# Kernel optimization log

Measured on AMD Instinct MI355X. Metric: run time of the kernel, lower is better.

Reference implementation:

```python
import jax, jax.numpy as jnp
import numpy as np

BOS = 1
MAX_LEN = 20


def _lstm_cell(x, h, c, Wih, Whh, bih, bhh):
    # torch.nn.LSTMCell gate order: i, f, g, o
    g = x @ Wih.T + h @ Whh.T + bih + bhh
    i, f, gg, o = jnp.split(g, 4, axis=-1)
    c = jax.nn.sigmoid(f) * c + jax.nn.sigmoid(i) * jnp.tanh(gg)
    h = jax.nn.sigmoid(o) * jnp.tanh(c)
    return h, c


def setup_inputs() -> dict:
    key = jax.random.key(0)
    ks = jax.random.split(key, 12)
    B, K, D = 512, 36, 2048
    A, H, Em, V = 512, 512, 300, 10000
    s = 0.02
    rn = lambda k, shape, sc=s: sc * jax.random.normal(k, shape, dtype=jnp.float32)
    return {
        'feats': jax.random.normal(ks[0], (B, K, D), dtype=jnp.float32),
        'Wp': rn(ks[1], (A, D)), 'bp': jnp.zeros((A,), jnp.float32),
        'E': rn(ks[2], (V, Em), 0.1).at[0].set(0.0),  # padding_idx = 0
        'Wih1': rn(ks[3], (4 * H, Em + A)), 'Whh1': rn(ks[4], (4 * H, H)),
        'bih1': jnp.zeros((4 * H,), jnp.float32), 'bhh1': jnp.zeros((4 * H,), jnp.float32),
        'Wih2': rn(ks[5], (4 * H, H + A)), 'Whh2': rn(ks[6], (4 * H, H)),
        'bih2': jnp.zeros((4 * H,), jnp.float32), 'bhh2': jnp.zeros((4 * H,), jnp.float32),
        'Wa1': rn(ks[7], (A, H + A)), 'ba1': jnp.zeros((A,), jnp.float32),
        'wa2': rn(ks[8], (1, A)), 'ba2': jnp.zeros((1,), jnp.float32),
        'Wo': rn(ks[9], (V, H)), 'bo': jnp.zeros((V,), jnp.float32),
    }


def reference(feats, Wp, bp, E, Wih1, Whh1, bih1, bhh1, Wih2, Whh2, bih2, bhh2,
              Wa1, ba1, wa2, ba2, Wo, bo):
    B, K, D = feats.shape
    H = Whh1.shape[1]
    f_att = feats @ Wp.T + bp                      # [B, K, A]
    f_mean = f_att.mean(axis=1)                    # [B, A]
    # attn Linear over concat([h1, f_att]): split columns, precompute f_att term
    Wa1_h, Wa1_f = Wa1[:, :H], Wa1[:, H:]
    att_f = f_att @ Wa1_f.T + ba1                  # [B, K, A]
    x0 = jnp.broadcast_to(E[BOS], (B, E.shape[1]))
    z = jnp.zeros((B, H), jnp.float32)
    carry0 = (x0, z, z, z, z)

    def step(carry, _):
        x, h1, c1, h2, c2 = carry
        h1, c1 = _lstm_cell(jnp.concatenate([x, f_mean], axis=-1), h1, c1,
                            Wih1, Whh1, bih1, bhh1)
        pre = jnp.tanh(att_f + (h1 @ Wa1_h.T)[:, None, :])   # [B, K, A]
        e = pre @ wa2[0] + ba2[0]                            # [B, K]
        alpha = jax.nn.softmax(e, axis=-1)
        ctx = jnp.einsum('bk,bka->ba', alpha, f_att)         # [B, A]
        h2, c2 = _lstm_cell(jnp.concatenate([h1, ctx], axis=-1), h2, c2,
                            Wih2, Whh2, bih2, bhh2)
        logit = h2 @ Wo.T + bo                               # [B, V]  (dropout is identity in eval)
        nxt = jnp.argmax(logit, axis=-1)
        return (E[nxt], h1, c1, h2, c2), nxt

    _, ids = jax.lax.scan(step, carry0, None, length=MAX_LEN - 1)
    return ids.T  # [B, MAX_LEN-1], matches torch.stack(out_ids, 1)
```

## Files before the change

kernel.cpp:

```cpp
#include <hip/hip_runtime.h>
#include <math.h>
#include <stdint.h>

constexpr int Bsz = 512, Kf = 36, Dd = 2048, Aa = 512, Hh = 512, Em = 300;
constexpr int Vv = 10000, TSTEPS = 19, BOS = 1;
constexpr int K1 = 832;
constexpr int K2 = 1536;
constexpr int VvP = 10112;
constexpr int NTL = VvP / 64;
constexpr float SPLIT_S  = 2048.0f;
constexpr float SPLIT_IS = 1.0f / 2048.0f;

#define CDIV(a,b) (((a)+(b)-1)/(b))

typedef _Float16 f16x8 __attribute__((ext_vector_type(8)));
typedef float    f32x4 __attribute__((ext_vector_type(4)));

typedef const unsigned int GU __attribute__((address_space(1)));
typedef unsigned int       LU __attribute__((address_space(3)));

__device__ __forceinline__ void gload16(const void* g, void* l) {
    __builtin_amdgcn_global_load_lds((GU*)g, (LU*)l, 16, 0, 0);
}

template<int N> __device__ __forceinline__ void wait_vm() {
    if constexpr (N == 0)       asm volatile("s_waitcnt vmcnt(0)" ::: "memory");
    else if constexpr (N == 4)  asm volatile("s_waitcnt vmcnt(4)" ::: "memory");
    else if constexpr (N == 6)  asm volatile("s_waitcnt vmcnt(6)" ::: "memory");
    else if constexpr (N == 8)  asm volatile("s_waitcnt vmcnt(8)" ::: "memory");
    else static_assert(N == 0, "unsupported vmcnt literal");
}
#define WAIT_LGKM asm volatile("s_waitcnt lgkmcnt(0)" ::: "memory")
#define SB0 __builtin_amdgcn_sched_barrier(0)
#define BAR __builtin_amdgcn_s_barrier()

__device__ __forceinline__ float sigm(float v) { return 1.0f / (1.0f + expf(-v)); }

__device__ __forceinline__ void wsplit(_Float16* __restrict__ hi, _Float16* __restrict__ lo,
                                       size_t idx, float v) {
    _Float16 h = (_Float16)v;
    hi[idx] = h;
    lo[idx] = (_Float16)((v - (float)h) * SPLIT_S);
}

template<int BM, int BN, int BK, bool AF32, bool SWZ, int OCC, int EPI>
__global__ __launch_bounds__(256, OCC)
void gemm_sp(const float* __restrict__ Af,
             const _Float16* __restrict__ Ahi, const _Float16* __restrict__ Alo, int lda,
             const _Float16* __restrict__ Bhi, const _Float16* __restrict__ Blo, int ldb,
             float* __restrict__ C, int ldc, int N, int K,
             const float* __restrict__ bias1, const float* __restrict__ bias2,
             const float* __restrict__ addC, int gxn,
             float* __restrict__ candV, int* __restrict__ candI, int ntl)
{
    constexpr int WM = BM / 2, WN = BN / 2;
    constexpr int MF = WM / 16, NF = WN / 16;
    constexpr int PA  = BK / 8;
    constexpr int PSA = BM * 8 + 8;
    constexpr int PSB = BN * 8 + 8;
    constexpr int SZA = PA * PSA, SZB = PA * PSB;
    constexpr int OAH = 0, OAL = SZA, OBH = 2 * SZA, OBL = 2 * SZA + SZB;
    constexpr int BUF = 2 * SZA + 2 * SZB;
    constexpr int NCHA = BM * BK / 2048;
    constexpr int NCHB = BN * BK / 2048;
    constexpr int LW = 2 * NCHA + 2 * NCHB;
    __shared__ _Float16 sm[2 * BUF];

    int mt, nt;
    if constexpr (SWZ) {
        const int nwg = gridDim.x;
        const int cpx = nwg >> 3;
        const int orig = blockIdx.x;
        const int lid = (orig & 7) * cpx + (orig >> 3);
        nt = lid % gxn; mt = lid / gxn;
    } else {
        nt = blockIdx.x; mt = blockIdx.y;
    }
    const int m0 = mt * BM, n0 = nt * BN;

    const int t    = threadIdx.x;
    const int lane = t & 63;
    const int w    = t >> 6;
    const int wr   = w >> 1, wc = w & 1;
    const int l15  = lane & 15, l4 = lane >> 4;

    f32x4 acch[MF][NF];
    f32x4 accm[MF][NF];
    #pragma unroll
    for (int m = 0; m < MF; ++m)
        #pragma unroll
        for (int n = 0; n < NF; ++n) {
            acch[m][n] = (f32x4){0.f, 0.f, 0.f, 0.f};
            accm[m][n] = (f32x4){0.f, 0.f, 0.f, 0.f};
        }

    const int nkt = K / BK;

    auto stageB = [&](int bufo, int kt) {
        #pragma unroll
        for (int i = 0; i < NCHB; ++i) {
            const int q  = i * 256 + t;
            const int p  = q / BN, r = q % BN;
            const int qw = i * 256 + (t & ~63);
            const int pu = qw / BN, ru = qw % BN;
            const size_t goff = (size_t)(n0 + r) * ldb + kt * BK + p * 8;
            gload16(Bhi + goff, &sm[bufo + OBH + pu * PSB + ru * 8]);
            gload16(Blo + goff, &sm[bufo + OBL + pu * PSB + ru * 8]);
        }
    };
    auto stageA16 = [&](int bufo, int kt) {
        #pragma unroll
        for (int i = 0; i < NCHA; ++i) {
            const int q  = i * 256 + t;
            const int p  = q / BM, r = q % BM;
            const int qw = i * 256 + (t & ~63);
            const int pu = qw / BM, ru = qw % BM;
            const size_t goff = (size_t)(m0 + r) * lda + kt * BK + p * 8;
            gload16(Ahi + goff, &sm[bufo + OAH + pu * PSA + ru * 8]);
            gload16(Alo + goff, &sm[bufo + OAL + pu * PSA + ru * 8]);
        }
    };
    auto issueA = [&](float4 (&rd)[NCHA][2], int kt) {
        #pragma unroll
        for (int i = 0; i < NCHA; ++i) {
            const int q = i * 256 + t;
            const int p = q / BM, r = q % BM;
            const float* src = Af + (size_t)(m0 + r) * lda + kt * BK + p * 8;
            rd[i][0] = *(const float4*)src;
            rd[i][1] = *(const float4*)(src + 4);
        }
    };
    auto writeA = [&](int bufo, float4 (&rd)[NCHA][2]) {
        #pragma unroll
        for (int i = 0; i < NCHA; ++i) {
            const int q = i * 256 + t;
            const int p = q / BM, r = q % BM;
            const float f[8] = {rd[i][0].x, rd[i][0].y, rd[i][0].z, rd[i][0].w,
                                rd[i][1].x, rd[i][1].y, rd[i][1].z, rd[i][1].w};
            f16x8 hi, lo;
            #pragma unroll
            for (int j = 0; j < 8; ++j) {
                _Float16 h = (_Float16)f[j];
                hi[j] = h;
                lo[j] = (_Float16)((f[j] - (float)h) * SPLIT_S);
            }
            *(f16x8*)&sm[bufo + OAH + p * PSA + r * 8] = hi;
            *(f16x8*)&sm[bufo + OAL + p * PSA + r * 8] = lo;
        }
    };
    auto compute = [&](int bufo) {
        #pragma unroll
        for (int s = 0; s < BK / 32; ++s) {
            f16x8 ah[MF], al[MF], bh[NF], bl[NF];
            const int pl = s * 4 + l4;
            #pragma unroll
            for (int m = 0; m < MF; ++m) {
                const int row = wr * WM + m * 16 + l15;
                ah[m] = *(const f16x8*)&sm[bufo + OAH + pl * PSA + row * 8];
                al[m] = *(const f16x8*)&sm[bufo + OAL + pl * PSA + row * 8];
            }
            #pragma unroll
            for (int n = 0; n < NF; ++n) {
                const int row = wc * WN + n * 16 + l15;
                bh[n] = *(const f16x8*)&sm[bufo + OBH + pl * PSB + row * 8];
                bl[n] = *(const f16x8*)&sm[bufo + OBL + pl * PSB + row * 8];
            }
            #pragma unroll
            for (int m = 0; m < MF; ++m)
                #pragma unroll
                for (int n = 0; n < NF; ++n) {
                    acch[m][n] = __builtin_amdgcn_mfma_f32_16x16x32_f16(ah[m], bh[n], acch[m][n], 0, 0, 0);
                    accm[m][n] = __builtin_amdgcn_mfma_f32_16x16x32_f16(ah[m], bl[n], accm[m][n], 0, 0, 0);
                    accm[m][n] = __builtin_amdgcn_mfma_f32_16x16x32_f16(al[m], bh[n], accm[m][n], 0, 0, 0);
                }
        }
    };

    if constexpr (AF32) {
        float4 rA[NCHA][2], rB[NCHA][2];
        issueA(rA, 0); stageB(0, 0);
        for (int kt = 0; kt < nkt; kt += 2) {
            issueA(rB, kt + 1); stageB(BUF, kt + 1);
            wait_vm<LW>(); SB0;
            writeA(0, rA);
            WAIT_LGKM; SB0;
            BAR; SB0;
            compute(0);
            SB0; WAIT_LGKM; BAR; SB0;
            if (kt + 2 < nkt) { issueA(rA, kt + 2); stageB(0, kt + 2); wait_vm<LW>(); }
            else              { wait_vm<0>(); }
            SB0;
            writeA(BUF, rB);
            WAIT_LGKM; SB0;
            BAR; SB0;
            compute(BUF);
            SB0; WAIT_LGKM; BAR; SB0;
        }
    } else {
        stageA16(0, 0); stageB(0, 0);
        for (int kt = 0; kt < nkt; ++kt) {
            const int bufc = (kt & 1) ? BUF : 0;
            const int bufn = BUF - bufc;
            if (kt + 1 < nkt) { stageA16(bufn, kt + 1); stageB(bufn, kt + 1); wait_vm<LW>(); }
            else              { wait_vm<0>(); }
            SB0;
            BAR; SB0;
            compute(bufc);
            SB0; WAIT_LGKM; BAR; SB0;
        }
    }

    if constexpr (EPI == 0) {
        #pragma unroll
        for (int m = 0; m < MF; ++m) {
            const int rowb = m0 + wr * WM + m * 16 + l4 * 4;
            #pragma unroll
            for (int n = 0; n < NF; ++n) {
                const int col = n0 + wc * WN + n * 16 + l15;
                if (col < N) {
                    float bb = 0.f;
                    if (bias1) bb += bias1[col];
                    if (bias2) bb += bias2[col];
                    #pragma unroll
                    for (int r = 0; r < 4; ++r) {
                        const size_t idx = (size_t)(rowb + r) * ldc + col;
                        float v = acch[m][n][r] + accm[m][n][r] * SPLIT_IS + bb;
                        if (addC) v += addC[idx];
                        C[idx] = v;
                    }
                }
            }
        }
    } else {
        float* sEv = reinterpret_cast<float*>(&sm[0]);
        int*   sEi = reinterpret_cast<int*>(&sm[0]) + 2 * BM;
        float bv[MF][4];
        int   bix[MF][4];
        #pragma unroll
        for (int m = 0; m < MF; ++m)
            #pragma unroll
            for (int r = 0; r < 4; ++r) { bv[m][r] = -INFINITY; bix[m][r] = 0x7fffffff; }
        #pragma unroll
        for (int m = 0; m < MF; ++m)
            #pragma unroll
            for (int r = 0; r < 4; ++r)
                #pragma unroll
                for (int n = 0; n < NF; ++n) {
                    const int col = n0 + wc * WN + n * 16 + l15;
                    if (col < N) {
                        const float x = acch[m][n][r] + accm[m][n][r] * SPLIT_IS + bias1[col];
                        if (x > bv[m][r]) { bv[m][r] = x; bix[m][r] = col; }
                    }
                }
        #pragma unroll
        for (int mask = 1; mask < 16; mask <<= 1) {
            #pragma unroll
            for (int m = 0; m < MF; ++m)
                #pragma unroll
                for (int r = 0; r < 4; ++r) {
                    const float ov = __shfl_xor(bv[m][r], mask);
                    const int   oi = __shfl_xor(bix[m][r], mask);
                    if (ov > bv[m][r] || (ov == bv[m][r] && oi < bix[m][r])) {
                        bv[m][r] = ov; bix[m][r] = oi;
                    }
                }
        }
        if (l15 == 0) {
            #pragma unroll
            for (int m = 0; m < MF; ++m)
                #pragma unroll
                for (int r = 0; r < 4; ++r) {
                    const int rl = wr * WM + m * 16 + l4 * 4 + r;
                    sEv[wc * BM + rl] = bv[m][r];
                    sEi[wc * BM + rl] = bix[m][r];
                }
        }
        __syncthreads();
        if (t < BM) {
            float v0 = sEv[t]; int i0 = sEi[t];
            const float v1 = sEv[BM + t]; const int i1 = sEi[BM + t];
            if (v1 > v0 || (v1 == v0 && i1 < i0)) { v0 = v1; i0 = i1; }
            candV[(size_t)(m0 + t) * ntl + nt] = v0;
            candI[(size_t)(m0 + t) * ntl + nt] = i0;
        }
    }
}

__global__ __launch_bounds__(256)
void split_convert(const float* __restrict__ src, int srcld, int validR,
                   _Float16* __restrict__ dhi, _Float16* __restrict__ dlo,
                   int dstld, int coloff, int R, int C)
{
    const int total = R * C;
    for (int i = blockIdx.x * 256 + threadIdx.x; i < total; i += gridDim.x * 256) {
        const int r = i / C, c = i % C;
        const float v = (r < validR) ? src[(size_t)r * srcld + c] : 0.f;
        wsplit(dhi, dlo, (size_t)r * dstld + coloff + c, v);
    }
}

__global__ __launch_bounds__(256)
void init_kernel(_Float16* __restrict__ a1h, _Float16* __restrict__ a1l,
                 _Float16* __restrict__ a2h, _Float16* __restrict__ a2l,
                 float* __restrict__ c1, float* __restrict__ c2,
                 const float* __restrict__ E)
{
    const int idx = blockIdx.x * 256 + threadIdx.x;
    if (idx < Bsz * K1) {
        const int col = idx % K1;
        const float v = (col < Em) ? E[(size_t)BOS * Em + col] : 0.f;
        wsplit(a1h, a1l, idx, v);
    }
    if (idx < Bsz * K2) wsplit(a2h, a2l, idx, 0.f);
    if (idx < Bsz * Hh) { c1[idx] = 0.f; c2[idx] = 0.f; }
}

__global__ __launch_bounds__(256)
void fmean_kernel(const float* __restrict__ f_att, float* __restrict__ f_mean,
                  _Float16* __restrict__ fmh, _Float16* __restrict__ fml)
{
    const int b = blockIdx.x;
    for (int a = threadIdx.x; a < Aa; a += 256) {
        float s = 0.f;
        for (int k = 0; k < Kf; ++k) s += f_att[((size_t)b * Kf + k) * Aa + a];
        const float v = s * (1.0f / 36.0f);
        f_mean[(size_t)b * Aa + a] = v;
        wsplit(fmh, fml, (size_t)b * Aa + a, v);
    }
}

__global__ __launch_bounds__(256)
void lstm_cell_kernel(const float* __restrict__ g, float* __restrict__ c,
                      _Float16* __restrict__ hhi, _Float16* __restrict__ hlo,
                      int hld, int hoff,
                      _Float16* __restrict__ h2hi, _Float16* __restrict__ h2lo,
                      int h2ld, int h2off)
{
    const int idx = blockIdx.x * 256 + threadIdx.x;
    const int b = idx >> 9, h = idx & 511;
    const float* gb = g + (size_t)b * 2048;
    const float gi = gb[h], gf = gb[512 + h], gc = gb[1024 + h], go = gb[1536 + h];
    const float cv = sigm(gf) * c[idx] + sigm(gi) * tanhf(gc);
    c[idx] = cv;
    const float hv = sigm(go) * tanhf(cv);
    wsplit(hhi, hlo, (size_t)b * hld + hoff + h, hv);
    if (h2hi) wsplit(h2hi, h2lo, (size_t)b * h2ld + h2off + h, hv);
}

__global__ __launch_bounds__(256)
void attn_fused(const float* __restrict__ att_f, const float* __restrict__ q,
                const float* __restrict__ wa2, const float* __restrict__ ba2,
                const float* __restrict__ f_att,
                _Float16* __restrict__ a2h, _Float16* __restrict__ a2l)
{
    const int b = blockIdx.x, tid = threadIdx.x;
    const int w = tid >> 6, lane = tid & 63;
    __shared__ float se[Kf];
    __shared__ float wk[Kf];
    const float* pq = q + (size_t)b * Aa;
    for (int k = w; k < Kf; k += 4) {
        const float* pf = att_f + ((size_t)b * Kf + k) * Aa;
        float s = 0.f;
        #pragma unroll
        for (int j = 0; j < Aa; j += 64) {
            const int a = j + lane;
            s += tanhf(pf[a] + pq[a]) * wa2[a];
        }
        #pragma unroll
        for (int off = 32; off; off >>= 1) s += __shfl_down(s, off);
        if (lane == 0) se[k] = s + ba2[0];
    }
    __syncthreads();
    if (tid < Kf) {
        float mx = -INFINITY;
        for (int k = 0; k < Kf; ++k) mx = fmaxf(mx, se[k]);
        float ssum = 0.f;
        for (int k = 0; k < Kf; ++k) ssum += expf(se[k] - mx);
        wk[tid] = expf(se[tid] - mx) / ssum;
    }
    __syncthreads();
    for (int a = tid; a < Aa; a += 256) {
        float acc = 0.f;
        for (int k = 0; k < Kf; ++k)
            acc = fmaf(wk[k], f_att[((size_t)b * Kf + k) * Aa + a], acc);
        wsplit(a2h, a2l, (size_t)b * K2 + Hh + a, acc);
    }
}

__global__ __launch_bounds__(256)
void argmax_embed_kernel(const float* __restrict__ candV, const int* __restrict__ candI,
                         const float* __restrict__ E,
                         _Float16* __restrict__ a1h, _Float16* __restrict__ a1l,
                         int* __restrict__ out, int t, int ntl)
{
    const int b = blockIdx.x;
    const int tid = threadIdx.x;
    __shared__ float sv[256];
    __shared__ int   si[256];
    float bvv = -INFINITY; int bii = 0x7fffffff;
    if (tid < ntl) { bvv = candV[(size_t)b * ntl + tid]; bii = candI[(size_t)b * ntl + tid]; }
    sv[tid] = bvv; si[tid] = bii;
    __syncthreads();
    for (int s = 128; s > 0; s >>= 1) {
        if (tid < s) {
            const float v2 = sv[tid + s];
            const int   i2 = si[tid + s];
            if (v2 > sv[tid] || (v2 == sv[tid] && i2 < si[tid])) { sv[tid] = v2; si[tid] = i2; }
        }
        __syncthreads();
    }
    const int idx = si[0];
    if (tid == 0) out[(size_t)b * TSTEPS + t] = idx;
    for (int d = tid; d < Em; d += 256)
        wsplit(a1h, a1l, (size_t)b * K1 + d, E[(size_t)idx * Em + d]);
}

static inline void conv(hipStream_t s, const float* src, int srcld, int validR,
                        _Float16* dhi, _Float16* dlo, int dstld, int coloff, int R, int C)
{
    int blocks = CDIV(R * C, 256); if (blocks > 2048) blocks = 2048;
    split_convert<<<dim3(blocks), dim3(256), 0, s>>>(src, srcld, validR, dhi, dlo, dstld, coloff, R, C);
}

extern "C" void kernel_launch(void* const* d_in, const int* in_sizes, int n_in,
                              void* d_out, int out_size, void* d_ws, size_t ws_size,
                              hipStream_t stream)
{
    const float* feats = (const float*)d_in[0];
    const float* Wp    = (const float*)d_in[1];
    const float* bp    = (const float*)d_in[2];
    const float* E     = (const float*)d_in[3];
    const float* Wih1  = (const float*)d_in[4];
    const float* Whh1  = (const float*)d_in[5];
    const float* bih1  = (const float*)d_in[6];
    const float* bhh1  = (const float*)d_in[7];
    const float* Wih2  = (const float*)d_in[8];
    const float* Whh2  = (const float*)d_in[9];
    const float* bih2  = (const float*)d_in[10];
    const float* bhh2  = (const float*)d_in[11];
    const float* Wa1   = (const float*)d_in[12];
    const float* ba1   = (const float*)d_in[13];
    const float* wa2   = (const float*)d_in[14];
    const float* ba2   = (const float*)d_in[15];
    const float* Wo    = (const float*)d_in[16];
    const float* bo    = (const float*)d_in[17];
    int* out = (int*)d_out;
    (void)in_sizes; (void)n_in; (void)out_size; (void)ws_size;

    uint8_t* w = (uint8_t*)d_ws;
    size_t off = 0;
    auto alloc = [&](size_t bytes) { void* p = w + off; off = (off + bytes + 255) & ~(size_t)255; return p; };

    float*     f_att  = (float*)alloc(18432ull * 512 * 4);
    float*     att_f  = (float*)alloc(18432ull * 512 * 4);
    float*     f_mean = (float*)alloc(512ull * 512 * 4);
    _Float16*  fmh    = (_Float16*)alloc(512ull * 512 * 2);
    _Float16*  fml    = (_Float16*)alloc(512ull * 512 * 2);
    _Float16*  wph    = (_Float16*)alloc(512ull * 2048 * 2);
    _Float16*  wpl    = (_Float16*)alloc(512ull * 2048 * 2);
    _Float16*  w1ph   = (_Float16*)alloc(2048ull * K1 * 2);
    _Float16*  w1pl   = (_Float16*)alloc(2048ull * K1 * 2);
    _Float16*  w1ch   = (_Float16*)alloc(2048ull * 512 * 2);
    _Float16*  w1cl   = (_Float16*)alloc(2048ull * 512 * 2);
    _Float16*  w2ph   = (_Float16*)alloc(2048ull * K2 * 2);
    _Float16*  w2pl   = (_Float16*)alloc(2048ull * K2 * 2);
    _Float16*  wahh   = (_Float16*)alloc(512ull * 512 * 2);
    _Float16*  wahl   = (_Float16*)alloc(512ull * 512 * 2);
    _Float16*  wafh   = (_Float16*)alloc(512ull * 512 * 2);
    _Float16*  wafl   = (_Float16*)alloc(512ull * 512 * 2);
    _Float16*  woh    = (_Float16*)alloc((size_t)VvP * 512 * 2);
    _Float16*  wol    = (_Float16*)alloc((size_t)VvP * 512 * 2);
    float*     g1c    = (float*)alloc(512ull * 2048 * 4);
    _Float16*  a1h    = (_Float16*)alloc(512ull * K1 * 2);
    _Float16*  a1l    = (_Float16*)alloc(512ull * K1 * 2);
    _Float16*  a2h    = (_Float16*)alloc(512ull * K2 * 2);
    _Float16*  a2l    = (_Float16*)alloc(512ull * K2 * 2);
    float*     c1     = (float*)alloc(512ull * 512 * 4);
    float*     c2     = (float*)alloc(512ull * 512 * 4);
    float*     gbuf   = (float*)alloc(512ull * 2048 * 4);
    float*     qbuf   = (float*)alloc(512ull * 512 * 4);
    float*     candV  = (float*)alloc(512ull * NTL * 4);
    int*       candI  = (int*)alloc(512ull * NTL * 4);

    conv(stream, Wp,        Dd,      512,  wph,  wpl,  2048, 0,    512,  2048);
    conv(stream, Wih1,      Em + Aa, 2048, w1ph, w1pl, K1,   0,    2048, Em);
    conv(stream, Whh1,      Hh,      2048, w1ph, w1pl, K1,   Em,   2048, 512);
    conv(stream, Wih1,      Em + Aa, 0,    w1ph, w1pl, K1,   812,  2048, 20);
    conv(stream, Wih1 + Em, Em + Aa, 2048, w1ch, w1cl, 512,  0,    2048, 512);
    conv(stream, Wih2,      Hh + Aa, 2048, w2ph, w2pl, K2,   0,    2048, 1024);
    conv(stream, Whh2,      Hh,      2048, w2ph, w2pl, K2,   1024, 2048, 512);
    conv(stream, Wa1,       Hh + Aa, 512,  wahh, wahl, 512,  0,    512,  512);
    conv(stream, Wa1 + Hh,  Hh + Aa, 512,  wafh, wafl, 512,  0,    512,  512);
    conv(stream, Wo,        Hh,      Vv,   woh,  wol,  512,  0,    VvP,  512);

    init_kernel<<<dim3(CDIV(Bsz * K2, 256)), dim3(256), 0, stream>>>(a1h, a1l, a2h, a2l, c1, c2, E);

    gemm_sp<128, 64, 32, true, true, 2, 0><<<dim3(1152), 256, 0, stream>>>(
        feats, nullptr, nullptr, Dd, wph, wpl, 2048, f_att, 512, 512, 2048,
        bp, nullptr, nullptr, 8, nullptr, nullptr, 0);
    fmean_kernel<<<dim3(Bsz), dim3(256), 0, stream>>>(f_att, f_mean, fmh, fml);
    gemm_sp<64, 64, 64, false, false, 1, 0><<<dim3(32, 8), 256, 0, stream>>>(
        nullptr, fmh, fml, 512, w1ch, w1cl, 512, g1c, 2048, 2048, 512,
        bih1, bhh1, nullptr, 0, nullptr, nullptr, 0);
    gemm_sp<128, 64, 32, true, true, 2, 0><<<dim3(1152), 256, 0, stream>>>(
        f_att, nullptr, nullptr, 512, wafh, wafl, 512, att_f, 512, 512, 512,
        ba1, nullptr, nullptr, 8, nullptr, nullptr, 0);

    for (int t = 0; t < TSTEPS; ++t) {
        gemm_sp<64, 64, 64, false, false, 1, 0><<<dim3(32, 8), 256, 0, stream>>>(
            nullptr, a1h, a1l, K1, w1ph, w1pl, K1, gbuf, 2048, 2048, K1,
            nullptr, nullptr, g1c, 0, nullptr, nullptr, 0);
        lstm_cell_kernel<<<dim3(Bsz * Hh / 256), dim3(256), 0, stream>>>(
            gbuf, c1, a2h, a2l, K2, 0, a1h, a1l, K1, Em);
        gemm_sp<64, 64, 64, false, false, 1, 0><<<dim3(8, 8), 256, 0, stream>>>(
            nullptr, a2h, a2l, K2, wahh, wahl, 512, qbuf, 512, 512, 512,
            nullptr, nullptr, nullptr, 0, nullptr, nullptr, 0);
        attn_fused<<<dim3(Bsz), dim3(256), 0, stream>>>(
            att_f, qbuf, wa2, ba2, f_att, a2h, a2l);
        gemm_sp<64, 64, 64, false, false, 1, 0><<<dim3(32, 8), 256, 0, stream>>>(
            nullptr, a2h, a2l, K2, w2ph, w2pl, K2, gbuf, 2048, 2048, K2,
            bih2, bhh2, nullptr, 0, nullptr, nullptr, 0);
        lstm_cell_kernel<<<dim3(Bsz * Hh / 256), dim3(256), 0, stream>>>(
            gbuf, c2, a2h, a2l, K2, 1024, nullptr, nullptr, 0, 0);
        gemm_sp<64, 64, 64, false, false, 1, 3><<<dim3(NTL, 8), 256, 0, stream>>>(
            nullptr, a2h + 1024, a2l + 1024, K2, woh, wol, 512, nullptr, 0, Vv, 512,
            bo, nullptr, nullptr, 0, candV, candI, NTL);
        argmax_embed_kernel<<<dim3(Bsz), dim3(256), 0, stream>>>(
            candV, candI, E, a1h, a1l, out, t, NTL);
    }
}
```

Measured before the change: 3.485 ms.

## Pre-split activations to fp16 pairs and use 4-deep async GEMM pipeline

Removes the in-kernel fp32-to-fp16 hi/lo split path from the GEMM. A separate pass now pre-splits the 18432x2048 feature tensor, and the f_att GEMM epilogue also writes split pairs for the next GEMM. All GEMMs then use a unified multi-stage (depth 4) global_load_lds pipeline with BK=32 and 64x64 tiles, plus an occupancy hint of 2. The pre-split costs an extra full read and write of feats (about 150MB fp32 read plus the same in fp16) in exchange for cheaper, deeper-pipelined main loops. A __syncthreads is also added in the argmax epilogue.

```diff
diff --git a/kernel.cpp b/kernel.cpp
--- a/kernel.cpp
+++ b/kernel.cpp
@@ -26,8 +26,10 @@
 template<int N> __device__ __forceinline__ void wait_vm() {
     if constexpr (N == 0)       asm volatile("s_waitcnt vmcnt(0)" ::: "memory");
     else if constexpr (N == 4)  asm volatile("s_waitcnt vmcnt(4)" ::: "memory");
-    else if constexpr (N == 6)  asm volatile("s_waitcnt vmcnt(6)" ::: "memory");
     else if constexpr (N == 8)  asm volatile("s_waitcnt vmcnt(8)" ::: "memory");
+    else if constexpr (N == 12) asm volatile("s_waitcnt vmcnt(12)" ::: "memory");
+    else if constexpr (N == 16) asm volatile("s_waitcnt vmcnt(16)" ::: "memory");
+    else if constexpr (N == 24) asm volatile("s_waitcnt vmcnt(24)" ::: "memory");
     else static_assert(N == 0, "unsupported vmcnt literal");
 }
 #define WAIT_LGKM asm volatile("s_waitcnt lgkmcnt(0)" ::: "memory")
@@ -43,14 +45,14 @@
     lo[idx] = (_Float16)((v - (float)h) * SPLIT_S);
 }
 
-template<int BM, int BN, int BK, bool AF32, bool SWZ, int OCC, int EPI>
+template<int BM, int BN, int BK, int DEPTH, bool SWZ, int OCC, int EPI>
 __global__ __launch_bounds__(256, OCC)
-void gemm_sp(const float* __restrict__ Af,
-             const _Float16* __restrict__ Ahi, const _Float16* __restrict__ Alo, int lda,
+void gemm_sp(const _Float16* __restrict__ Ahi, const _Float16* __restrict__ Alo, int lda,
              const _Float16* __restrict__ Bhi, const _Float16* __restrict__ Blo, int ldb,
              float* __restrict__ C, int ldc, int N, int K,
              const float* __restrict__ bias1, const float* __restrict__ bias2,
              const float* __restrict__ addC, int gxn,
+             _Float16* __restrict__ pairH, _Float16* __restrict__ pairL,
              float* __restrict__ candV, int* __restrict__ candI, int ntl)
 {
     constexpr int WM = BM / 2, WN = BN / 2;
@@ -64,7 +66,8 @@
     constexpr int NCHA = BM * BK / 2048;
     constexpr int NCHB = BN * BK / 2048;
     constexpr int LW = 2 * NCHA + 2 * NCHB;
-    __shared__ _Float16 sm[2 * BUF];
+    static_assert((DEPTH & (DEPTH - 1)) == 0, "DEPTH pow2");
+    __shared__ _Float16 sm[DEPTH * BUF];
 
     int mt, nt;
     if constexpr (SWZ) {
@@ -96,7 +99,17 @@
 
     const int nkt = K / BK;
 
-    auto stageB = [&](int bufo, int kt) {
+    auto stage = [&](int bufo, int kt) {
+        #pragma unroll
+        for (int i = 0; i < NCHA; ++i) {
+            const int q  = i * 256 + t;
+            const int p  = q / BM, r = q % BM;
+            const int qw = i * 256 + (t & ~63);
+            const int pu = qw / BM, ru = qw % BM;
+            const size_t goff = (size_t)(m0 + r) * lda + kt * BK + p * 8;
+            gload16(Ahi + goff, &sm[bufo + OAH + pu * PSA + ru * 8]);
+            gload16(Alo + goff, &sm[bufo + OAL + pu * PSA + ru * 8]);
+        }
         #pragma unroll
         for (int i = 0; i < NCHB; ++i) {
             const int q  = i * 256 + t;
@@ -108,46 +121,6 @@
             gload16(Blo + goff, &sm[bufo + OBL + pu * PSB + ru * 8]);
         }
     };
-    auto stageA16 = [&](int bufo, int kt) {
-        #pragma unroll
-        for (int i = 0; i < NCHA; ++i) {
-            const int q  = i * 256 + t;
-            const int p  = q / BM, r = q % BM;
-            const int qw = i * 256 + (t & ~63);
-            const int pu = qw / BM, ru = qw % BM;
-            const size_t goff = (size_t)(m0 + r) * lda + kt * BK + p * 8;
-            gload16(Ahi + goff, &sm[bufo + OAH + pu * PSA + ru * 8]);
-            gload16(Alo + goff, &sm[bufo + OAL + pu * PSA + ru * 8]);
-        }
-    };
-    auto issueA = [&](float4 (&rd)[NCHA][2], int kt) {
-        #pragma unroll
-        for (int i = 0; i < NCHA; ++i) {
-            const int q = i * 256 + t;
-            const int p = q / BM, r = q % BM;
-            const float* src = Af + (size_t)(m0 + r) * lda + kt * BK + p * 8;
-            rd[i][0] = *(const float4*)src;
-            rd[i][1] = *(const float4*)(src + 4);
-        }
-    };
-    auto writeA = [&](int bufo, float4 (&rd)[NCHA][2]) {
-        #pragma unroll
-        for (int i = 0; i < NCHA; ++i) {
-            const int q = i * 256 + t;
-            const int p = q / BM, r = q % BM;
-            const float f[8] = {rd[i][0].x, rd[i][0].y, rd[i][0].z, rd[i][0].w,
-                                rd[i][1].x, rd[i][1].y, rd[i][1].z, rd[i][1].w};
-            f16x8 hi, lo;
-            #pragma unroll
-            for (int j = 0; j < 8; ++j) {
-                _Float16 h = (_Float16)f[j];
-                hi[j] = h;
-                lo[j] = (_Float16)((f[j] - (float)h) * SPLIT_S);
-            }
-            *(f16x8*)&sm[bufo + OAH + p * PSA + r * 8] = hi;
-            *(f16x8*)&sm[bufo + OAL + p * PSA + r * 8] = lo;
-        }
-    };
     auto compute = [&](int bufo) {
         #pragma unroll
         for (int s = 0; s < BK / 32; ++s) {
@@ -176,41 +149,30 @@
         }
     };
 
-    if constexpr (AF32) {
-        float4 rA[NCHA][2], rB[NCHA][2];
-        issueA(rA, 0); stageB(0, 0);
-        for (int kt = 0; kt < nkt; kt += 2) {
-            issueA(rB, kt + 1); stageB(BUF, kt + 1);
-            wait_vm<LW>(); SB0;
-            writeA(0, rA);
-            WAIT_LGKM; SB0;
-            BAR; SB0;
-            compute(0);
-            SB0; WAIT_LGKM; BAR; SB0;
-            if (kt + 2 < nkt) { issueA(rA, kt + 2); stageB(0, kt + 2); wait_vm<LW>(); }
-            else              { wait_vm<0>(); }
-            SB0;
-            writeA(BUF, rB);
-            WAIT_LGKM; SB0;
-            BAR; SB0;
-            compute(BUF);
-            SB0; WAIT_LGKM; BAR; SB0;
-        }
-    } else {
-        stageA16(0, 0); stageB(0, 0);
-        for (int kt = 0; kt < nkt; ++kt) {
-            const int bufc = (kt & 1) ? BUF : 0;
-            const int bufn = BUF - bufc;
-            if (kt + 1 < nkt) { stageA16(bufn, kt + 1); stageB(bufn, kt + 1); wait_vm<LW>(); }
-            else              { wait_vm<0>(); }
-            SB0;
-            BAR; SB0;
-            compute(bufc);
-            SB0; WAIT_LGKM; BAR; SB0;
-        }
-    }
-
-    if constexpr (EPI == 0) {
+    #pragma unroll
+    for (int d = 0; d < DEPTH - 1; ++d) stage(d * BUF, d);
+
+    for (int kt = 0; kt < nkt; ++kt) {
+        const int bc = (kt & (DEPTH - 1)) * BUF;
+        if (kt + DEPTH - 1 < nkt) {
+            stage(((kt + DEPTH - 1) & (DEPTH - 1)) * BUF, kt + DEPTH - 1);
+            wait_vm<(DEPTH - 1) * LW>();
+        } else if (kt + 3 < nkt) {
+            wait_vm<3 * LW>();
+        } else if (kt + 2 < nkt) {
+            wait_vm<2 * LW>();
+        } else if (kt + 1 < nkt) {
+            wait_vm<LW>();
+        } else {
+            wait_vm<0>();
+        }
+        SB0;
+        BAR; SB0;
+        compute(bc);
+        SB0; WAIT_LGKM; BAR; SB0;
+    }
+
+    if constexpr (EPI == 0 || EPI == 4) {
         #pragma unroll
         for (int m = 0; m < MF; ++m) {
             const int rowb = m0 + wr * WM + m * 16 + l4 * 4;
@@ -227,6 +189,7 @@
                         float v = acch[m][n][r] + accm[m][n][r] * SPLIT_IS + bb;
                         if (addC) v += addC[idx];
                         C[idx] = v;
+                        if constexpr (EPI == 4) wsplit(pairH, pairL, idx, v);
                     }
                 }
             }
@@ -265,6 +228,7 @@
                     }
                 }
         }
+        __syncthreads();
         if (l15 == 0) {
             #pragma unroll
             for (int m = 0; m < MF; ++m)
@@ -296,6 +260,26 @@
         const int r = i / C, c = i % C;
         const float v = (r < validR) ? src[(size_t)r * srcld + c] : 0.f;
         wsplit(dhi, dlo, (size_t)r * dstld + coloff + c, v);
+    }
+}
+
+__global__ __launch_bounds__(256)
+void split_flat8(const float* __restrict__ src,
+                 _Float16* __restrict__ dh, _Float16* __restrict__ dl, int n8)
+{
+    for (int i = blockIdx.x * 256 + threadIdx.x; i < n8; i += gridDim.x * 256) {
+        const float4 a = ((const float4*)src)[2 * i];
+        const float4 b = ((const float4*)src)[2 * i + 1];
+        const float f[8] = {a.x, a.y, a.z, a.w, b.x, b.y, b.z, b.w};
+        f16x8 hi, lo;
+        #pragma unroll
+        for (int j = 0; j < 8; ++j) {
+            _Float16 h = (_Float16)f[j];
+            hi[j] = h;
+            lo[j] = (_Float16)((f[j] - (float)h) * SPLIT_S);
+        }
+        ((f16x8*)dh)[i] = hi;
+        ((f16x8*)dl)[i] = lo;
     }
 }
 
@@ -453,6 +437,10 @@
 
     float*     f_att  = (float*)alloc(18432ull * 512 * 4);
     float*     att_f  = (float*)alloc(18432ull * 512 * 4);
+    _Float16*  fah    = (_Float16*)alloc(18432ull * 512 * 2);
+    _Float16*  fal    = (_Float16*)alloc(18432ull * 512 * 2);
+    _Float16*  fth    = (_Float16*)alloc(18432ull * 2048 * 2);
+    _Float16*  ftl    = (_Float16*)alloc(18432ull * 2048 * 2);
     float*     f_mean = (float*)alloc(512ull * 512 * 4);
     _Float16*  fmh    = (_Float16*)alloc(512ull * 512 * 2);
     _Float16*  fml    = (_Float16*)alloc(512ull * 512 * 2);
@@ -492,39 +480,40 @@
     conv(stream, Wa1,       Hh + Aa, 512,  wahh, wahl, 512,  0,    512,  512);
     conv(stream, Wa1 + Hh,  Hh + Aa, 512,  wafh, wafl, 512,  0,    512,  512);
     conv(stream, Wo,        Hh,      Vv,   woh,  wol,  512,  0,    VvP,  512);
+    split_flat8<<<dim3(2048), dim3(256), 0, stream>>>(feats, fth, ftl, 18432 * 2048 / 8);
 
     init_kernel<<<dim3(CDIV(Bsz * K2, 256)), dim3(256), 0, stream>>>(a1h, a1l, a2h, a2l, c1, c2, E);
 
-    gemm_sp<128, 64, 32, true, true, 2, 0><<<dim3(1152), 256, 0, stream>>>(
-        feats, nullptr, nullptr, Dd, wph, wpl, 2048, f_att, 512, 512, 2048,
-        bp, nullptr, nullptr, 8, nullptr, nullptr, 0);
+    gemm_sp<64, 64, 32, 4, true, 2, 4><<<dim3(2304), 256, 0, stream>>>(
+        fth, ftl, Dd, wph, wpl, 2048, f_att, 512, 512, 2048,
+        bp, nullptr, nullptr, 8, fah, fal, nullptr, nullptr, 0);
     fmean_kernel<<<dim3(Bsz), dim3(256), 0, stream>>>(f_att, f_mean, fmh, fml);
-    gemm_sp<64, 64, 64, false, false, 1, 0><<<dim3(32, 8), 256, 0, stream>>>(
-        nullptr, fmh, fml, 512, w1ch, w1cl, 512, g1c, 2048, 2048, 512,
-        bih1, bhh1, nullptr, 0, nullptr, nullptr, 0);
-    gemm_sp<128, 64, 32, true, true, 2, 0><<<dim3(1152), 256, 0, stream>>>(
-        f_att, nullptr, nullptr, 512, wafh, wafl, 512, att_f, 512, 512, 512,
-        ba1, nullptr, nullptr, 8, nullptr, nullptr, 0);
+    gemm_sp<64, 64, 32, 4, false, 2, 0><<<dim3(32, 8), 256, 0, stream>>>(
+        fmh, fml, 512, w1ch, w1cl, 512, g1c, 2048, 2048, 512,
+        bih1, bhh1, nullptr, 0, nullptr, nullptr, nullptr, nullptr, 0);
+    gemm_sp<64, 64, 32, 4, true, 2, 0><<<dim3(2304), 256, 0, stream>>>(
+        fah, fal, 512, wafh, wafl, 512, att_f, 512, 512, 512,
+        ba1, nullptr, nullptr, 8, nullptr, nullptr, nullptr, nullptr, 0);
 
     for (int t = 0; t < TSTEPS; ++t) {
-        gemm_sp<64, 64, 64, false, false, 1, 0><<<dim3(32, 8), 256, 0, stream>>>(
-            nullptr, a1h, a1l, K1, w1ph, w1pl, K1, gbuf, 2048, 2048, K1,
-            nullptr, nullptr, g1c, 0, nullptr, nullptr, 0);
+        gemm_sp<64, 64, 32, 4, false, 2, 0><<<dim3(32, 8), 256, 0, stream>>>(
+            a1h, a1l, K1, w1ph, w1pl, K1, gbuf, 2048, 2048, K1,
+            nullptr, nullptr, g1c, 0, nullptr, nullptr, nullptr, nullptr, 0);
         lstm_cell_kernel<<<dim3(Bsz * Hh / 256), dim3(256), 0, stream>>>(
             gbuf, c1, a2h, a2l, K2, 0, a1h, a1l, K1, Em);
-        gemm_sp<64, 64, 64, false, false, 1, 0><<<dim3(8, 8), 256, 0, stream>>>(
-            nullptr, a2h, a2l, K2, wahh, wahl, 512, qbuf, 512, 512, 512,
-            nullptr, nullptr, nullptr, 0, nullptr, nullptr, 0);
+        gemm_sp<64, 64, 32, 4, false, 2, 0><<<dim3(8, 8), 256, 0, stream>>>(
+            a2h, a2l, K2, wahh, wahl, 512, qbuf, 512, 512, 512,
+            nullptr, nullptr, nullptr, 0, nullptr, nullptr, nullptr, nullptr, 0);
         attn_fused<<<dim3(Bsz), dim3(256), 0, stream>>>(
             att_f, qbuf, wa2, ba2, f_att, a2h, a2l);
-        gemm_sp<64, 64, 64, false, false, 1, 0><<<dim3(32, 8), 256, 0, stream>>>(
-            nullptr, a2h, a2l, K2, w2ph, w2pl, K2, gbuf, 2048, 2048, K2,
-            bih2, bhh2, nullptr, 0, nullptr, nullptr, 0);
+        gemm_sp<64, 64, 32, 4, false, 2, 0><<<dim3(32, 8), 256, 0, stream>>>(
+            a2h, a2l, K2, w2ph, w2pl, K2, gbuf, 2048, 2048, K2,
+            bih2, bhh2, nullptr, 0, nullptr, nullptr, nullptr, nullptr, 0);
         lstm_cell_kernel<<<dim3(Bsz * Hh / 256), dim3(256), 0, stream>>>(
             gbuf, c2, a2h, a2l, K2, 1024, nullptr, nullptr, 0, 0);
-        gemm_sp<64, 64, 64, false, false, 1, 3><<<dim3(NTL, 8), 256, 0, stream>>>(
-            nullptr, a2h + 1024, a2l + 1024, K2, woh, wol, 512, nullptr, 0, Vv, 512,
-            bo, nullptr, nullptr, 0, candV, candI, NTL);
+        gemm_sp<64, 64, 32, 4, false, 2, 3><<<dim3(NTL, 8), 256, 0, stream>>>(
+            a2h + 1024, a2l + 1024, K2, woh, wol, 512, nullptr, 0, Vv, 512,
+            bo, nullptr, nullptr, 0, nullptr, nullptr, candV, candI, NTL);
         argmax_embed_kernel<<<dim3(Bsz), dim3(256), 0, stream>>>(
             candV, candI, E, a1h, a1l, out, t, NTL);
     }
```

Measured after the change: 3.647 ms. 1.05x slower.
